# Optimization experiments

Hardware: AMD Instinct MI355X
Metric: run time of the kernel (lower is better)

Reference implementation:

```python
import jax, jax.numpy as jnp
import numpy as np

NUM_HEADS = 32
NUM_KV_HEADS = 8
HEAD_DIM = 128


def rotate_half(x):
    half = x.shape[-1] // 2
    return jnp.concatenate([-x[..., half:], x[..., :half]], axis=-1)


def setup_inputs() -> dict:
    key = jax.random.key(0)
    ks = jax.random.split(key, 7)
    B, S, H = 2, 2048, 4096
    hidden_states = jax.random.normal(ks[0], (B, S, H), dtype=jnp.float32)
    # rope tables built from real frequencies for realism
    inv_freq = 1.0 / (10000.0 ** (jnp.arange(0, HEAD_DIM, 2, dtype=jnp.float32) / HEAD_DIM))
    pos = jnp.arange(S, dtype=jnp.float32)
    freqs = pos[:, None] * inv_freq[None, :]            # [S, HEAD_DIM//2]
    emb = jnp.concatenate([freqs, freqs], axis=-1)      # [S, HEAD_DIM]
    cos = jnp.broadcast_to(jnp.cos(emb)[None], (B, S, HEAD_DIM)).astype(jnp.float32)
    sin = jnp.broadcast_to(jnp.sin(emb)[None], (B, S, HEAD_DIM)).astype(jnp.float32)
    scale = 0.02
    wq = jax.random.normal(ks[1], (NUM_HEADS * HEAD_DIM, H), dtype=jnp.float32) * scale
    wk = jax.random.normal(ks[2], (NUM_KV_HEADS * HEAD_DIM, H), dtype=jnp.float32) * scale
    wv = jax.random.normal(ks[3], (NUM_KV_HEADS * HEAD_DIM, H), dtype=jnp.float32) * scale
    wo = jax.random.normal(ks[4], (H, NUM_HEADS * HEAD_DIM), dtype=jnp.float32) * scale
    return {"hidden_states": hidden_states, "cos": cos, "sin": sin,
            "wq": wq, "wk": wk, "wv": wv, "wo": wo}


def reference(hidden_states, cos, sin, wq, wk, wv, wo):
    B, S, H = hidden_states.shape
    groups = NUM_HEADS // NUM_KV_HEADS
    scaling = HEAD_DIM ** -0.5

    # QKV projections (nn.Linear, no bias -> x @ W^T)
    q = (hidden_states @ wq.T).reshape(B, S, NUM_HEADS, HEAD_DIM).transpose(0, 2, 1, 3)     # [B,Hq,S,D]
    k = (hidden_states @ wk.T).reshape(B, S, NUM_KV_HEADS, HEAD_DIM).transpose(0, 2, 1, 3)  # [B,Hk,S,D]
    v = (hidden_states @ wv.T).reshape(B, S, NUM_KV_HEADS, HEAD_DIM).transpose(0, 2, 1, 3)  # [B,Hk,S,D]

    # RoPE (HF apply_rotary_pos_emb: cos/sin unsqueezed over head axis)
    c = cos[:, None, :, :]  # [B,1,S,D]
    s = sin[:, None, :, :]
    q = q * c + rotate_half(q) * s
    k = k * c + rotate_half(k) * s

    # GQA: broadcast each KV head to its group of query heads
    k = jnp.repeat(k, groups, axis=1)  # [B,Hq,S,D]
    v = jnp.repeat(v, groups, axis=1)

    # causal SDPA
    scores = jnp.einsum('bhqd,bhkd->bhqk', q, k) * scaling
    causal = jnp.tril(jnp.ones((S, S), dtype=bool))
    neg = jnp.finfo(scores.dtype).min
    scores = jnp.where(causal[None, None], scores, neg)
    probs = jax.nn.softmax(scores, axis=-1)
    attn = jnp.einsum('bhqk,bhkd->bhqd', probs, v)      # [B,Hq,S,D]

    # merge heads + output projection
    attn = attn.transpose(0, 2, 1, 3).reshape(B, S, NUM_HEADS * HEAD_DIM)
    return attn @ wo.T
```

## Files before the change

### kernel.cpp

```cpp
#include <hip/hip_runtime.h>
#include <stdint.h>

typedef __bf16 bf16_t;
typedef __bf16 bf16x8 __attribute__((ext_vector_type(8)));
typedef __bf16 bf16x4 __attribute__((ext_vector_type(4)));
typedef __bf16 bf16x2 __attribute__((ext_vector_type(2)));
typedef float f32x4 __attribute__((ext_vector_type(4)));

#define S_LEN 2048
#define NH 32
#define NKV 8
#define HD 128
#define B_SZ 2
#define HID 4096
#define QKV_N 6144
#define INFF __builtin_inff()
#define QSCALE (0.08838834764831845f * 1.4426950408889634f)

__device__ __forceinline__ void gload_lds16(const void* g, void* l) {
    __builtin_amdgcn_global_load_lds(
        (const __attribute__((address_space(1))) void*)(uintptr_t)g,
        (__attribute__((address_space(3))) void*)(uint32_t)(uintptr_t)l,
        16, 0, 0);
}

__global__ __launch_bounds__(256) void f2b_kernel(const float4* __restrict__ in,
                                                  bf16x4* __restrict__ out, int n4) {
    int i = blockIdx.x * blockDim.x + threadIdx.x;
    if (i >= n4) return;
    float4 v = in[i];
    bf16x4 o = {(bf16_t)v.x, (bf16_t)v.y, (bf16_t)v.z, (bf16_t)v.w};
    out[i] = o;
}

#define SLOT_E 16384

#define GTILE(T, STAGE, VMW) do {                                                         \
    const int _sb = ((T) & 3) * SLOT_E;                                                   \
    const int _ss = (((T) + 3) & 3) * SLOT_E;                                             \
    bf16x8 af[8], bfr[2], bfs[2];                                                         \
    _Pragma("unroll") for (int i = 0; i < 8; ++i)                                         \
        af[i] = *(const bf16x8*)&lds[_sb + offA[i]];                                      \
    bfr[0] = *(const bf16x8*)&lds[_sb + 8192 + offB[0]];                                  \
    bfr[1] = *(const bf16x8*)&lds[_sb + 8192 + offB[1]];                                  \
    if (STAGE) {                                                                          \
        gload_lds16(sA0, &lds[_ss + ldsO0]); gload_lds16(sA1, &lds[_ss + ldsO1]);         \
        sA0 += 32; sA1 += 32;                                                             \
    }                                                                                     \
    __builtin_amdgcn_s_setprio(1);                                                        \
    _Pragma("unroll") for (int i = 0; i < 8; ++i) {                                       \
        acc[i][0] = __builtin_amdgcn_mfma_f32_16x16x32_bf16(af[i], bfr[0], acc[i][0], 0, 0, 0); \
        acc[i][1] = __builtin_amdgcn_mfma_f32_16x16x32_bf16(af[i], bfr[1], acc[i][1], 0, 0, 0); \
    }                                                                                     \
    __builtin_amdgcn_s_setprio(0);                                                        \
    bfs[0] = *(const bf16x8*)&lds[_sb + 8192 + offB[2]];                                  \
    bfs[1] = *(const bf16x8*)&lds[_sb + 8192 + offB[3]];                                  \
    if (STAGE) {                                                                          \
        gload_lds16(sB0, &lds[_ss + 8192 + ldsO0]); gload_lds16(sB1, &lds[_ss + 8192 + ldsO1]); \
        sB0 += 32; sB1 += 32;                                                             \
    }                                                                                     \
    __builtin_amdgcn_s_setprio(1);                                                        \
    _Pragma("unroll") for (int i = 0; i < 8; ++i) {                                       \
        acc[i][2] = __builtin_amdgcn_mfma_f32_16x16x32_bf16(af[i], bfs[0], acc[i][2], 0, 0, 0); \
        acc[i][3] = __builtin_amdgcn_mfma_f32_16x16x32_bf16(af[i], bfs[1], acc[i][3], 0, 0, 0); \
    }                                                                                     \
    __builtin_amdgcn_s_setprio(0);                                                        \
    if ((VMW) == 8)      asm volatile("s_waitcnt vmcnt(8)" ::: "memory");                 \
    else if ((VMW) == 4) asm volatile("s_waitcnt vmcnt(4)" ::: "memory");                 \
    else if ((VMW) == 0) asm volatile("s_waitcnt vmcnt(0)" ::: "memory");                 \
    __builtin_amdgcn_s_barrier();                                                         \
} while (0)

template<bool F32OUT>
__global__ __launch_bounds__(512) void gemm256(const bf16_t* __restrict__ A,
                                               const bf16_t* __restrict__ W,
                                               void* __restrict__ C0,
                                               void* __restrict__ C1,
                                               int ld0, int ld1,
                                               int Nloc, int ldAW, int Kloc) {
    __shared__ __align__(16) bf16_t lds[4 * SLOT_E];
    const int tid = threadIdx.x;
    const int lane = tid & 63;
    const int w = tid >> 6;
    const int wm = w >> 2, wn = w & 3;
    const int l15 = lane & 15, lg = lane >> 4;

    const int z = blockIdx.y;
    void* Cv = z ? C1 : C0;
    const int ldC = z ? ld1 : ld0;
    const int kOff = z * Kloc;

    const int nbx = Nloc >> 8;
    const int cpx = gridDim.x >> 3;
    const int bid = blockIdx.x;
    const int bid2 = (bid & 7) * cpx + (bid >> 3);
    const int m0 = (bid2 / nbx) * 256;
    const int n0 = (bid2 % nbx) * 256;

    const int c0 = tid, c1 = 512 + tid;
    const int rA0 = c0 >> 2, ch0 = (c0 & 3) ^ ((rA0 >> 1) & 3);
    const int rA1 = c1 >> 2, ch1 = (c1 & 3) ^ ((rA1 >> 1) & 3);
    const bf16_t* sA0 = A + (size_t)(m0 + rA0) * ldAW + kOff + ch0 * 8;
    const bf16_t* sA1 = A + (size_t)(m0 + rA1) * ldAW + kOff + ch1 * 8;
    const bf16_t* sB0 = W + (size_t)(n0 + rA0) * ldAW + kOff + ch0 * 8;
    const bf16_t* sB1 = W + (size_t)(n0 + rA1) * ldAW + kOff + ch1 * 8;
    const int ldsO0 = c0 * 8, ldsO1 = c1 * 8;

    int offA[8], offB[4];
    #pragma unroll
    for (int i = 0; i < 8; ++i) {
        int row = wm * 128 + i * 16 + l15;
        offA[i] = row * 32 + ((lg ^ ((row >> 1) & 3)) * 8);
    }
    #pragma unroll
    for (int j = 0; j < 4; ++j) {
        int row = wn * 64 + j * 16 + l15;
        offB[j] = row * 32 + ((lg ^ ((row >> 1) & 3)) * 8);
    }

    #pragma unroll
    for (int tt = 0; tt < 3; ++tt) {
        const int ss = tt * SLOT_E;
        gload_lds16(sA0, &lds[ss + ldsO0]); gload_lds16(sA1, &lds[ss + ldsO1]);
        gload_lds16(sB0, &lds[ss + 8192 + ldsO0]); gload_lds16(sB1, &lds[ss + 8192 + ldsO1]);
        sA0 += 32; sA1 += 32; sB0 += 32; sB1 += 32;
    }
    asm volatile("s_waitcnt vmcnt(8)" ::: "memory");
    __builtin_amdgcn_s_barrier();

    f32x4 acc[8][4] = {};
    const int NT = Kloc >> 5;
    int t = 0;
    for (; t < NT - 3; ++t) GTILE(t, true, 8);
    GTILE(NT - 3, false, 4);
    GTILE(NT - 2, false, 0);
    GTILE(NT - 1, false, -1);

    #pragma unroll
    for (int i = 0; i < 8; ++i)
        #pragma unroll
        for (int jn = 0; jn < 4; ++jn)
            #pragma unroll
            for (int r = 0; r < 4; ++r) {
                int m = m0 + wm * 128 + i * 16 + lg * 4 + r;
                int n = n0 + wn * 64 + jn * 16 + l15;
                float v = acc[i][jn][r];
                if (F32OUT) ((float*)Cv)[(size_t)m * ldC + n] = v;
                else        ((bf16_t*)Cv)[(size_t)m * ldC + n] = (bf16_t)v;
            }
}

__global__ __launch_bounds__(256) void rope_fuse(bf16_t* __restrict__ QKV,
                                                 const bf16_t* __restrict__ P1,
                                                 const float* __restrict__ cosb,
                                                 const float* __restrict__ sinb) {
    int tid = blockIdx.x * blockDim.x + threadIdx.x;
    int d = tid & 63;
    int hg = (tid >> 6) % 48;
    int bs = tid / (64 * 48);
    bf16_t* rowp;
    float x1, x2, posc = 1.f;
    if (hg < 32) {
        rowp = QKV + (size_t)bs * QKV_N + hg * HD;
        x1 = (float)rowp[d];
        x2 = (float)rowp[d + 64];
        posc = QSCALE;
    } else if (hg < 40) {
        int col = HID + (hg - 32) * HD;
        rowp = QKV + (size_t)bs * QKV_N + col;
        const bf16_t* pp = P1 + (size_t)bs * 2048 + (col - HID);
        x1 = (float)rowp[d] + (float)pp[d];
        x2 = (float)rowp[d + 64] + (float)pp[d + 64];
    } else {
        int col = HID + NKV * HD + (hg - 40) * HD;
        rowp = QKV + (size_t)bs * QKV_N + col;
        const bf16_t* pp = P1 + (size_t)bs * 2048 + (col - HID);
        rowp[d]      = (bf16_t)((float)rowp[d]      + (float)pp[d]);
        rowp[d + 64] = (bf16_t)((float)rowp[d + 64] + (float)pp[d + 64]);
        return;
    }
    float c1 = cosb[(size_t)bs * HD + d];
    float s1 = sinb[(size_t)bs * HD + d];
    float c2 = cosb[(size_t)bs * HD + d + 64];
    float s2 = sinb[(size_t)bs * HD + d + 64];
    rowp[d]      = (bf16_t)((x1 * c1 - x2 * s1) * posc);
    rowp[d + 64] = (bf16_t)((x2 * c2 + x1 * s2) * posc);
}

#define PITCH_P 72

__global__ __launch_bounds__(512) void attn_fwd(const bf16_t* __restrict__ QKV,
                                                bf16_t* __restrict__ O) {
    __shared__ __align__(16) bf16_t Kl[2][64 * 128];
    __shared__ __align__(16) bf16_t Vt[2][128 * 64];
    __shared__ __align__(16) bf16_t Pl[8][2][16 * PITCH_P];
    const int tid = threadIdx.x;
    const int lane = tid & 63;
    const int w = tid >> 6;
    const int l15 = lane & 15, lg = lane >> 4;
    const int pr = blockIdx.x, kvh = blockIdx.y, b = blockIdx.z;
    const int h = kvh * 4 + (w & 3);
    const int rg = w >> 2;

    int krow[2], kch[2];
    #pragma unroll
    for (int jj = 0; jj < 2; ++jj) { int q = jj * 512 + tid; krow[jj] = q >> 4; kch[jj] = q & 15; }
    const int k0v = (tid & 31) * 2;
    const int d0 = (tid >> 5) * 8;
    const int vci = k0v >> 3;
    const int vsub = k0v & 7;

    const bf16_t* Kb0 = QKV + (size_t)(b * S_LEN) * QKV_N + HID + kvh * HD;
    const bf16_t* Vb0 = QKV + (size_t)(b * S_LEN) * QKV_N + HID + NKV * HD + kvh * HD;
    bf16_t* Pl0 = Pl[w][0];
    bf16_t* Pl1 = Pl[w][1];

    for (int t = 0; t < 2; ++t) {
        const int qt = (t == 0) ? pr : (31 - pr);
        const int q0 = qt * 64;
        const int qb0 = q0 + rg * 32;
        const int qb1 = qb0 + 16;
        const int qrow0 = qb0 + l15, qrow1 = qb1 + l15;

        bf16x8 qf0[4], qf1[4];
        {
            const bf16_t* qp0 = QKV + (size_t)(b * S_LEN + qrow0) * QKV_N + h * HD;
            const bf16_t* qp1 = QKV + (size_t)(b * S_LEN + qrow1) * QKV_N + h * HD;
            #pragma unroll
            for (int c = 0; c < 4; ++c) {
                qf0[c] = *(const bf16x8*)&qp0[c * 32 + lg * 8];
                qf1[c] = *(const bf16x8*)&qp1[c * 32 + lg * 8];
            }
        }

        f32x4 acc0[8] = {}, acc1[8] = {};
        float mr0 = -INFF, lr0 = 0.f, mr1 = -INFF, lr1 = 0.f;
        const int nsteps = qt + 1;

        bf16x8 kst[2], vst[2];
        #pragma unroll
        for (int jj = 0; jj < 2; ++jj)
            kst[jj] = *(const bf16x8*)&Kb0[(size_t)krow[jj] * QKV_N + kch[jj] * 8];
        vst[0] = *(const bf16x8*)&Vb0[(size_t)(k0v + 0) * QKV_N + d0];
        vst[1] = *(const bf16x8*)&Vb0[(size_t)(k0v + 1) * QKV_N + d0];

        for (int st = 0; st < nsteps; ++st) {
            const int k0 = st * 64;
            const int p = st & 1;
            #pragma unroll
            for (int jj = 0; jj < 2; ++jj)
                *(bf16x8*)&Kl[p][krow[jj] * 128 + ((kch[jj] ^ (krow[jj] & 7)) * 8)] = kst[jj];
            #pragma unroll
            for (int j = 0; j < 8; ++j) {
                bf16x2 v2 = { vst[0][j], vst[1][j] };
                *(bf16x2*)&Vt[p][(d0 + j) * 64 + ((vci ^ j) << 3) + vsub] = v2;
            }
            __syncthreads();
            if (st + 1 < nsteps) {
                const bf16_t* Kb = Kb0 + (size_t)(k0 + 64) * QKV_N;
                const bf16_t* Vb = Vb0 + (size_t)(k0 + 64) * QKV_N;
                #pragma unroll
                for (int jj = 0; jj < 2; ++jj)
                    kst[jj] = *(const bf16x8*)&Kb[(size_t)krow[jj] * QKV_N + kch[jj] * 8];
                vst[0] = *(const bf16x8*)&Vb[(size_t)(k0v + 0) * QKV_N + d0];
                vst[1] = *(const bf16x8*)&Vb[(size_t)(k0v + 1) * QKV_N + d0];
            }
            f32x4 s0[4], s1[4];
            __builtin_amdgcn_s_setprio(1);
            #pragma unroll
            for (int nt = 0; nt < 4; ++nt) {
                s0[nt] = (f32x4){0.f, 0.f, 0.f, 0.f};
                s1[nt] = (f32x4){0.f, 0.f, 0.f, 0.f};
                const int row = nt * 16 + l15;
                const int rb = row * 128, key = row & 7;
                #pragma unroll
                for (int c = 0; c < 4; ++c) {
                    bf16x8 kf = *(const bf16x8*)&Kl[p][rb + (((c * 4 + lg) ^ key) * 8)];
                    s0[nt] = __builtin_amdgcn_mfma_f32_16x16x32_bf16(kf, qf0[c], s0[nt], 0, 0, 0);
                    s1[nt] = __builtin_amdgcn_mfma_f32_16x16x32_bf16(kf, qf1[c], s1[nt], 0, 0, 0);
                }
            }
            __builtin_amdgcn_s_setprio(0);
            if (k0 + 63 > qb0) {
                #pragma unroll
                for (int nt = 0; nt < 4; ++nt)
                    #pragma unroll
                    for (int r = 0; r < 4; ++r) {
                        int k = k0 + nt * 16 + lg * 4 + r;
                        if (k > qrow0) s0[nt][r] = -INFF;
                    }
            }
            if (k0 + 63 > qb1) {
                #pragma unroll
                for (int nt = 0; nt < 4; ++nt)
                    #pragma unroll
                    for (int r = 0; r < 4; ++r) {
                        int k = k0 + nt * 16 + lg * 4 + r;
                        if (k > qrow1) s1[nt][r] = -INFF;
                    }
            }
            {
                float ma = fmaxf(fmaxf(s0[0][0], s0[0][1]), fmaxf(s0[0][2], s0[0][3]));
                float mb = fmaxf(fmaxf(s0[1][0], s0[1][1]), fmaxf(s0[1][2], s0[1][3]));
                float mc = fmaxf(fmaxf(s0[2][0], s0[2][1]), fmaxf(s0[2][2], s0[2][3]));
                float md = fmaxf(fmaxf(s0[3][0], s0[3][1]), fmaxf(s0[3][2], s0[3][3]));
                float mx = fmaxf(fmaxf(ma, mb), fmaxf(mc, md));
                mx = fmaxf(mx, __shfl_xor(mx, 16));
                mx = fmaxf(mx, __shfl_xor(mx, 32));
                const bool nodefer = !__all(mx <= mr0 + 11.5f);
                const float mn = nodefer ? fmaxf(mr0, mx) : mr0;
                float sc = 1.f;
                if (nodefer) sc = exp2f(mr0 - mn);
                float rsum = 0.f;
                #pragma unroll
                for (int nt = 0; nt < 4; ++nt) {
                    float e0 = exp2f(s0[nt][0] - mn), e1 = exp2f(s0[nt][1] - mn);
                    float e2 = exp2f(s0[nt][2] - mn), e3 = exp2f(s0[nt][3] - mn);
                    s0[nt][0] = e0; s0[nt][1] = e1; s0[nt][2] = e2; s0[nt][3] = e3;
                    rsum += (e0 + e1) + (e2 + e3);
                }
                rsum += __shfl_xor(rsum, 16);
                rsum += __shfl_xor(rsum, 32);
                if (nodefer) { lr0 = lr0 * sc + rsum; mr0 = mn; }
                else         { lr0 += rsum; }
                #pragma unroll
                for (int nt = 0; nt < 4; ++nt) {
                    bf16x4 pk = {(bf16_t)s0[nt][0], (bf16_t)s0[nt][1], (bf16_t)s0[nt][2], (bf16_t)s0[nt][3]};
                    *(bf16x4*)&Pl0[l15 * PITCH_P + nt * 16 + lg * 4] = pk;
                }
                if (nodefer) {
                    float scb[4];
                    #pragma unroll
                    for (int r = 0; r < 4; ++r) scb[r] = __shfl(sc, lg * 4 + r);
                    #pragma unroll
                    for (int nt2 = 0; nt2 < 8; ++nt2)
                        #pragma unroll
                        for (int r = 0; r < 4; ++r) acc0[nt2][r] *= scb[r];
                }
            }
            {
                float ma = fmaxf(fmaxf(s1[0][0], s1[0][1]), fmaxf(s1[0][2], s1[0][3]));
                float mb = fmaxf(fmaxf(s1[1][0], s1[1][1]), fmaxf(s1[1][2], s1[1][3]));
                float mc = fmaxf(fmaxf(s1[2][0], s1[2][1]), fmaxf(s1[2][2], s1[2][3]));
                float md = fmaxf(fmaxf(s1[3][0], s1[3][1]), fmaxf(s1[3][2], s1[3][3]));
                float mx = fmaxf(fmaxf(ma, mb), fmaxf(mc, md));
                mx = fmaxf(mx, __shfl_xor(mx, 16));
                mx = fmaxf(mx, __shfl_xor(mx, 32));
                const bool nodefer = !__all(mx <= mr1 + 11.5f);
                const float mn = nodefer ? fmaxf(mr1, mx) : mr1;
                float sc = 1.f;
                if (nodefer) sc = exp2f(mr1 - mn);
                float rsum = 0.f;
                #pragma unroll
                for (int nt = 0; nt < 4; ++nt) {
                    float e0 = exp2f(s1[nt][0] - mn), e1 = exp2f(s1[nt][1] - mn);
                    float e2 = exp2f(s1[nt][2] - mn), e3 = exp2f(s1[nt][3] - mn);
                    s1[nt][0] = e0; s1[nt][1] = e1; s1[nt][2] = e2; s1[nt][3] = e3;
                    rsum += (e0 + e1) + (e2 + e3);
                }
                rsum += __shfl_xor(rsum, 16);
                rsum += __shfl_xor(rsum, 32);
                if (nodefer) { lr1 = lr1 * sc + rsum; mr1 = mn; }
                else         { lr1 += rsum; }
                #pragma unroll
                for (int nt = 0; nt < 4; ++nt) {
                    bf16x4 pk = {(bf16_t)s1[nt][0], (bf16_t)s1[nt][1], (bf16_t)s1[nt][2], (bf16_t)s1[nt][3]};
                    *(bf16x4*)&Pl1[l15 * PITCH_P + nt * 16 + lg * 4] = pk;
                }
                if (nodefer) {
                    float scb[4];
                    #pragma unroll
                    for (int r = 0; r < 4; ++r) scb[r] = __shfl(sc, lg * 4 + r);
                    #pragma unroll
                    for (int nt2 = 0; nt2 < 8; ++nt2)
                        #pragma unroll
                        for (int r = 0; r < 4; ++r) acc1[nt2][r] *= scb[r];
                }
            }
            __builtin_amdgcn_s_setprio(1);
            #pragma unroll
            for (int kc = 0; kc < 2; ++kc) {
                bf16x8 pf0 = *(const bf16x8*)&Pl0[l15 * PITCH_P + kc * 32 + lg * 8];
                bf16x8 pf1 = *(const bf16x8*)&Pl1[l15 * PITCH_P + kc * 32 + lg * 8];
                #pragma unroll
                for (int nt2 = 0; nt2 < 8; ++nt2) {
                    const int drow = nt2 * 16 + l15;
                    bf16x8 vf = *(const bf16x8*)&Vt[p][drow * 64 + (((kc * 4 + lg) ^ (drow & 7)) << 3)];
                    acc0[nt2] = __builtin_amdgcn_mfma_f32_16x16x32_bf16(pf0, vf, acc0[nt2], 0, 0, 0);
                    acc1[nt2] = __builtin_amdgcn_mfma_f32_16x16x32_bf16(pf1, vf, acc1[nt2], 0, 0, 0);
                }
            }
            __builtin_amdgcn_s_setprio(0);
        }
        float lb0[4], lb1[4];
        #pragma unroll
        for (int r = 0; r < 4; ++r) {
            lb0[r] = __builtin_amdgcn_rcpf(__shfl(lr0, lg * 4 + r));
            lb1[r] = __builtin_amdgcn_rcpf(__shfl(lr1, lg * 4 + r));
        }
        #pragma unroll
        for (int nt2 = 0; nt2 < 8; ++nt2)
            #pragma unroll
            for (int r = 0; r < 4; ++r) {
                int d = nt2 * 16 + l15;
                int qa = qb0 + lg * 4 + r;
                int qb = qb1 + lg * 4 + r;
                O[((size_t)(b * S_LEN + qa)) * (NH * HD) + h * HD + d] = (bf16_t)(acc0[nt2][r] * lb0[r]);
                O[((size_t)(b * S_LEN + qb)) * (NH * HD) + h * HD + d] = (bf16_t)(acc1[nt2][r] * lb1[r]);
            }
        __syncthreads();
    }
}

extern "C" void kernel_launch(void* const* d_in, const int* in_sizes, int n_in,
                              void* d_out, int out_size, void* d_ws, size_t ws_size,
                              hipStream_t stream) {
    const float* hs   = (const float*)d_in[0];
    const float* cosb = (const float*)d_in[1];
    const float* sinb = (const float*)d_in[2];
    const float* wq   = (const float*)d_in[3];
    const float* wk   = (const float*)d_in[4];
    const float* wv   = (const float*)d_in[5];
    const float* wo   = (const float*)d_in[6];
    float* out = (float*)d_out;

    const size_t NHS = (size_t)B_SZ * S_LEN * HID;
    const size_t NQKVW = (size_t)QKV_N * HID;
    size_t need = (NHS * 3 + NQKVW * 2) * sizeof(bf16_t);
    if (ws_size < need) return;

    bf16_t* p = (bf16_t*)d_ws;
    bf16_t* hsb  = p; p += NHS;
    bf16_t* wqkv = p; p += NQKVW;
    bf16_t* wob  = p; p += NHS;
    bf16_t* QKVb = p; p += NQKVW;
    bf16_t* Ab   = p; p += NHS;
    bf16_t* P1   = Ab;

    auto cvt = [&](const float* src, bf16_t* dst, size_t n) {
        int n4 = (int)(n / 4);
        f2b_kernel<<<(n4 + 255) / 256, 256, 0, stream>>>((const float4*)src, (bf16x4*)dst, n4);
    };
    cvt(hs, hsb, NHS);
    cvt(wq, wqkv, NHS);
    cvt(wk, wqkv + (size_t)HID * HID, (size_t)NKV * HD * HID);
    cvt(wv, wqkv + (size_t)(HID + NKV * HD) * HID, (size_t)NKV * HD * HID);
    cvt(wo, wob, NHS);

    gemm256<false><<<dim3(256, 1), 512, 0, stream>>>(hsb, wqkv, QKVb, QKVb,
                                                     QKV_N, QKV_N, 4096, HID, HID);
    gemm256<false><<<dim3(128, 2), 512, 0, stream>>>(hsb, wqkv + (size_t)HID * HID,
                                                     QKVb + HID, P1,
                                                     QKV_N, 2048, 2048, HID, 2048);

    int rf_threads = B_SZ * S_LEN * 48 * 64;
    rope_fuse<<<rf_threads / 256, 256, 0, stream>>>(QKVb, P1, cosb, sinb);

    attn_fwd<<<dim3(16, NKV, B_SZ), 512, 0, stream>>>(QKVb, Ab);

    gemm256<true><<<dim3(256, 1), 512, 0, stream>>>(Ab, wob, out, out,
                                                    HID, HID, HID, HID, HID);
}
```

Baseline: 519.1 us.

## Split attention blocks into half-GQA-group blocks and XOR-swizzle the P tile

Each attention block now serves two of the four query heads in a KV group with 256 threads instead of all four with 512. The grid doubles to 512 blocks. Each thread loads more K/V rows per step, and V is transposed into LDS with 4-wide stores. The P scratch tile drops its padded pitch in favour of an XOR swizzle, which cuts LDS use per block. The goal is more blocks and better occupancy on the CUs, at the cost of each K/V tile being loaded twice (once per half-group).

```diff
diff --git a/kernel.cpp b/kernel.cpp
--- a/kernel.cpp
+++ b/kernel.cpp
@@ -187,26 +187,27 @@
     rowp[d + 64] = (bf16_t)((x2 * c2 + x1 * s2) * posc);
 }
 
-#define PITCH_P 72
-
-__global__ __launch_bounds__(512) void attn_fwd(const bf16_t* __restrict__ QKV,
+__global__ __launch_bounds__(256) void attn_fwd(const bf16_t* __restrict__ QKV,
                                                 bf16_t* __restrict__ O) {
     __shared__ __align__(16) bf16_t Kl[2][64 * 128];
     __shared__ __align__(16) bf16_t Vt[2][128 * 64];
-    __shared__ __align__(16) bf16_t Pl[8][2][16 * PITCH_P];
+    __shared__ __align__(16) bf16_t Pl[4][2][16 * 64];
     const int tid = threadIdx.x;
     const int lane = tid & 63;
     const int w = tid >> 6;
     const int l15 = lane & 15, lg = lane >> 4;
-    const int pr = blockIdx.x, kvh = blockIdx.y, b = blockIdx.z;
-    const int h = kvh * 4 + (w & 3);
-    const int rg = w >> 2;
-
-    int krow[2], kch[2];
+    const int pr = blockIdx.x;
+    const int kvh = blockIdx.y >> 1, hs = blockIdx.y & 1;
+    const int b = blockIdx.z;
+    const int h = kvh * 4 + hs * 2 + (w & 1);
+    const int rg = w >> 1;
+    const int pkey = l15 & 7;
+
+    int krow[4], kch[4];
     #pragma unroll
-    for (int jj = 0; jj < 2; ++jj) { int q = jj * 512 + tid; krow[jj] = q >> 4; kch[jj] = q & 15; }
-    const int k0v = (tid & 31) * 2;
-    const int d0 = (tid >> 5) * 8;
+    for (int jj = 0; jj < 4; ++jj) { int q = jj * 256 + tid; krow[jj] = q >> 4; kch[jj] = q & 15; }
+    const int k0v = (tid & 15) * 4;
+    const int d0 = (tid >> 4) * 8;
     const int vci = k0v >> 3;
     const int vsub = k0v & 7;
 
@@ -237,33 +238,35 @@
         float mr0 = -INFF, lr0 = 0.f, mr1 = -INFF, lr1 = 0.f;
         const int nsteps = qt + 1;
 
-        bf16x8 kst[2], vst[2];
+        bf16x8 kst[4], vst[4];
         #pragma unroll
-        for (int jj = 0; jj < 2; ++jj)
+        for (int jj = 0; jj < 4; ++jj)
             kst[jj] = *(const bf16x8*)&Kb0[(size_t)krow[jj] * QKV_N + kch[jj] * 8];
-        vst[0] = *(const bf16x8*)&Vb0[(size_t)(k0v + 0) * QKV_N + d0];
-        vst[1] = *(const bf16x8*)&Vb0[(size_t)(k0v + 1) * QKV_N + d0];
+        #pragma unroll
+        for (int j2 = 0; j2 < 4; ++j2)
+            vst[j2] = *(const bf16x8*)&Vb0[(size_t)(k0v + j2) * QKV_N + d0];
 
         for (int st = 0; st < nsteps; ++st) {
             const int k0 = st * 64;
             const int p = st & 1;
             #pragma unroll
-            for (int jj = 0; jj < 2; ++jj)
+            for (int jj = 0; jj < 4; ++jj)
                 *(bf16x8*)&Kl[p][krow[jj] * 128 + ((kch[jj] ^ (krow[jj] & 7)) * 8)] = kst[jj];
             #pragma unroll
             for (int j = 0; j < 8; ++j) {
-                bf16x2 v2 = { vst[0][j], vst[1][j] };
-                *(bf16x2*)&Vt[p][(d0 + j) * 64 + ((vci ^ j) << 3) + vsub] = v2;
+                bf16x4 cvec = { vst[0][j], vst[1][j], vst[2][j], vst[3][j] };
+                *(bf16x4*)&Vt[p][(d0 + j) * 64 + ((vci ^ j) << 3) + vsub] = cvec;
             }
             __syncthreads();
             if (st + 1 < nsteps) {
                 const bf16_t* Kb = Kb0 + (size_t)(k0 + 64) * QKV_N;
                 const bf16_t* Vb = Vb0 + (size_t)(k0 + 64) * QKV_N;
                 #pragma unroll
-                for (int jj = 0; jj < 2; ++jj)
+                for (int jj = 0; jj < 4; ++jj)
                     kst[jj] = *(const bf16x8*)&Kb[(size_t)krow[jj] * QKV_N + kch[jj] * 8];
-                vst[0] = *(const bf16x8*)&Vb[(size_t)(k0v + 0) * QKV_N + d0];
-                vst[1] = *(const bf16x8*)&Vb[(size_t)(k0v + 1) * QKV_N + d0];
+                #pragma unroll
+                for (int j2 = 0; j2 < 4; ++j2)
+                    vst[j2] = *(const bf16x8*)&Vb[(size_t)(k0v + j2) * QKV_N + d0];
             }
             f32x4 s0[4], s1[4];
             __builtin_amdgcn_s_setprio(1);
@@ -326,7 +329,8 @@
                 #pragma unroll
                 for (int nt = 0; nt < 4; ++nt) {
                     bf16x4 pk = {(bf16_t)s0[nt][0], (bf16_t)s0[nt][1], (bf16_t)s0[nt][2], (bf16_t)s0[nt][3]};
-                    *(bf16x4*)&Pl0[l15 * PITCH_P + nt * 16 + lg * 4] = pk;
+                    const int cw = nt * 2 + (lg >> 1);
+                    *(bf16x4*)&Pl0[l15 * 64 + ((cw ^ pkey) * 8) + (lg & 1) * 4] = pk;
                 }
                 if (nodefer) {
                     float scb[4];
@@ -365,7 +369,8 @@
                 #pragma unroll
                 for (int nt = 0; nt < 4; ++nt) {
                     bf16x4 pk = {(bf16_t)s1[nt][0], (bf16_t)s1[nt][1], (bf16_t)s1[nt][2], (bf16_t)s1[nt][3]};
-                    *(bf16x4*)&Pl1[l15 * PITCH_P + nt * 16 + lg * 4] = pk;
+                    const int cw = nt * 2 + (lg >> 1);
+                    *(bf16x4*)&Pl1[l15 * 64 + ((cw ^ pkey) * 8) + (lg & 1) * 4] = pk;
                 }
                 if (nodefer) {
                     float scb[4];
@@ -380,8 +385,8 @@
             __builtin_amdgcn_s_setprio(1);
             #pragma unroll
             for (int kc = 0; kc < 2; ++kc) {
-                bf16x8 pf0 = *(const bf16x8*)&Pl0[l15 * PITCH_P + kc * 32 + lg * 8];
-                bf16x8 pf1 = *(const bf16x8*)&Pl1[l15 * PITCH_P + kc * 32 + lg * 8];
+                bf16x8 pf0 = *(const bf16x8*)&Pl0[l15 * 64 + (((kc * 4 + lg) ^ pkey) * 8)];
+                bf16x8 pf1 = *(const bf16x8*)&Pl1[l15 * 64 + (((kc * 4 + lg) ^ pkey) * 8)];
                 #pragma unroll
                 for (int nt2 = 0; nt2 < 8; ++nt2) {
                     const int drow = nt2 * 16 + l15;
@@ -456,7 +461,7 @@
     int rf_threads = B_SZ * S_LEN * 48 * 64;
     rope_fuse<<<rf_threads / 256, 256, 0, stream>>>(QKVb, P1, cosb, sinb);
 
-    attn_fwd<<<dim3(16, NKV, B_SZ), 512, 0, stream>>>(QKVb, Ab);
+    attn_fwd<<<dim3(16, 16, B_SZ), 256, 0, stream>>>(QKVb, Ab);
 
     gemm256<true><<<dim3(256, 1), 512, 0, stream>>>(Ab, wob, out, out,
                                                     HID, HID, HID, HID, HID);
```

New measurement: 587.7 us. +13.2%, slower.

## Split attention blocks by head pair and shrink KV tile to 32 keys

Applied to the files above, without the earlier changes.

Each attention workgroup now covers two of the four query heads sharing a KV head, so the grid doubles to 512 blocks of 256 threads. The KV step shrinks from 64 to 32 keys, halving the K, V and P shared-memory tiles, and the swizzle patterns are adjusted to the narrower tiles. The aim is more blocks and smaller LDS per block for better occupancy and CU fill. In exchange each K/V tile is loaded by two blocks instead of one, and twice as many loop steps each carry a barrier and softmax bookkeeping.

```diff
diff --git a/kernel.cpp b/kernel.cpp
--- a/kernel.cpp
+++ b/kernel.cpp
@@ -187,26 +187,28 @@
     rowp[d + 64] = (bf16_t)((x2 * c2 + x1 * s2) * posc);
 }
 
-#define PITCH_P 72
-
-__global__ __launch_bounds__(512) void attn_fwd(const bf16_t* __restrict__ QKV,
+#define PITCH_P 40
+
+__global__ __launch_bounds__(256) void attn_fwd(const bf16_t* __restrict__ QKV,
                                                 bf16_t* __restrict__ O) {
-    __shared__ __align__(16) bf16_t Kl[2][64 * 128];
-    __shared__ __align__(16) bf16_t Vt[2][128 * 64];
-    __shared__ __align__(16) bf16_t Pl[8][2][16 * PITCH_P];
+    __shared__ __align__(16) bf16_t Kl[2][32 * 128];
+    __shared__ __align__(16) bf16_t Vt[2][128 * 32];
+    __shared__ __align__(16) bf16_t Pl[4][2][16 * PITCH_P];
     const int tid = threadIdx.x;
     const int lane = tid & 63;
     const int w = tid >> 6;
     const int l15 = lane & 15, lg = lane >> 4;
-    const int pr = blockIdx.x, kvh = blockIdx.y, b = blockIdx.z;
-    const int h = kvh * 4 + (w & 3);
-    const int rg = w >> 2;
+    const int pr = blockIdx.x;
+    const int kvh = blockIdx.y >> 1, hs = blockIdx.y & 1;
+    const int b = blockIdx.z;
+    const int h = kvh * 4 + hs * 2 + (w & 1);
+    const int rg = w >> 1;
 
     int krow[2], kch[2];
     #pragma unroll
-    for (int jj = 0; jj < 2; ++jj) { int q = jj * 512 + tid; krow[jj] = q >> 4; kch[jj] = q & 15; }
-    const int k0v = (tid & 31) * 2;
-    const int d0 = (tid >> 5) * 8;
+    for (int jj = 0; jj < 2; ++jj) { int q = jj * 256 + tid; krow[jj] = q >> 4; kch[jj] = q & 15; }
+    const int k0v = (tid & 15) * 2;
+    const int d0 = (tid >> 4) * 8;
     const int vci = k0v >> 3;
     const int vsub = k0v & 7;
 
@@ -235,7 +237,7 @@
 
         f32x4 acc0[8] = {}, acc1[8] = {};
         float mr0 = -INFF, lr0 = 0.f, mr1 = -INFF, lr1 = 0.f;
-        const int nsteps = qt + 1;
+        const int nsteps = 2 * qt + 2;
 
         bf16x8 kst[2], vst[2];
         #pragma unroll
@@ -245,7 +247,7 @@
         vst[1] = *(const bf16x8*)&Vb0[(size_t)(k0v + 1) * QKV_N + d0];
 
         for (int st = 0; st < nsteps; ++st) {
-            const int k0 = st * 64;
+            const int k0 = st * 32;
             const int p = st & 1;
             #pragma unroll
             for (int jj = 0; jj < 2; ++jj)
@@ -253,22 +255,23 @@
             #pragma unroll
             for (int j = 0; j < 8; ++j) {
                 bf16x2 v2 = { vst[0][j], vst[1][j] };
-                *(bf16x2*)&Vt[p][(d0 + j) * 64 + ((vci ^ j) << 3) + vsub] = v2;
+                const int d = d0 + j;
+                *(bf16x2*)&Vt[p][d * 32 + ((vci ^ (d & 3)) * 8) + vsub] = v2;
             }
             __syncthreads();
             if (st + 1 < nsteps) {
-                const bf16_t* Kb = Kb0 + (size_t)(k0 + 64) * QKV_N;
-                const bf16_t* Vb = Vb0 + (size_t)(k0 + 64) * QKV_N;
+                const bf16_t* Kb = Kb0 + (size_t)(k0 + 32) * QKV_N;
+                const bf16_t* Vb = Vb0 + (size_t)(k0 + 32) * QKV_N;
                 #pragma unroll
                 for (int jj = 0; jj < 2; ++jj)
                     kst[jj] = *(const bf16x8*)&Kb[(size_t)krow[jj] * QKV_N + kch[jj] * 8];
                 vst[0] = *(const bf16x8*)&Vb[(size_t)(k0v + 0) * QKV_N + d0];
                 vst[1] = *(const bf16x8*)&Vb[(size_t)(k0v + 1) * QKV_N + d0];
             }
-            f32x4 s0[4], s1[4];
+            f32x4 s0[2], s1[2];
             __builtin_amdgcn_s_setprio(1);
             #pragma unroll
-            for (int nt = 0; nt < 4; ++nt) {
+            for (int nt = 0; nt < 2; ++nt) {
                 s0[nt] = (f32x4){0.f, 0.f, 0.f, 0.f};
                 s1[nt] = (f32x4){0.f, 0.f, 0.f, 0.f};
                 const int row = nt * 16 + l15;
@@ -281,18 +284,18 @@
                 }
             }
             __builtin_amdgcn_s_setprio(0);
-            if (k0 + 63 > qb0) {
-                #pragma unroll
-                for (int nt = 0; nt < 4; ++nt)
+            if (k0 + 31 > qb0) {
+                #pragma unroll
+                for (int nt = 0; nt < 2; ++nt)
                     #pragma unroll
                     for (int r = 0; r < 4; ++r) {
                         int k = k0 + nt * 16 + lg * 4 + r;
                         if (k > qrow0) s0[nt][r] = -INFF;
                     }
             }
-            if (k0 + 63 > qb1) {
-                #pragma unroll
-                for (int nt = 0; nt < 4; ++nt)
+            if (k0 + 31 > qb1) {
+                #pragma unroll
+                for (int nt = 0; nt < 2; ++nt)
                     #pragma unroll
                     for (int r = 0; r < 4; ++r) {
                         int k = k0 + nt * 16 + lg * 4 + r;
@@ -302,9 +305,7 @@
             {
                 float ma = fmaxf(fmaxf(s0[0][0], s0[0][1]), fmaxf(s0[0][2], s0[0][3]));
                 float mb = fmaxf(fmaxf(s0[1][0], s0[1][1]), fmaxf(s0[1][2], s0[1][3]));
-                float mc = fmaxf(fmaxf(s0[2][0], s0[2][1]), fmaxf(s0[2][2], s0[2][3]));
-                float md = fmaxf(fmaxf(s0[3][0], s0[3][1]), fmaxf(s0[3][2], s0[3][3]));
-                float mx = fmaxf(fmaxf(ma, mb), fmaxf(mc, md));
+                float mx = fmaxf(ma, mb);
                 mx = fmaxf(mx, __shfl_xor(mx, 16));
                 mx = fmaxf(mx, __shfl_xor(mx, 32));
                 const bool nodefer = !__all(mx <= mr0 + 11.5f);
@@ -313,7 +314,7 @@
                 if (nodefer) sc = exp2f(mr0 - mn);
                 float rsum = 0.f;
                 #pragma unroll
-                for (int nt = 0; nt < 4; ++nt) {
+                for (int nt = 0; nt < 2; ++nt) {
                     float e0 = exp2f(s0[nt][0] - mn), e1 = exp2f(s0[nt][1] - mn);
                     float e2 = exp2f(s0[nt][2] - mn), e3 = exp2f(s0[nt][3] - mn);
                     s0[nt][0] = e0; s0[nt][1] = e1; s0[nt][2] = e2; s0[nt][3] = e3;
@@ -324,7 +325,7 @@
                 if (nodefer) { lr0 = lr0 * sc + rsum; mr0 = mn; }
                 else         { lr0 += rsum; }
                 #pragma unroll
-                for (int nt = 0; nt < 4; ++nt) {
+                for (int nt = 0; nt < 2; ++nt) {
                     bf16x4 pk = {(bf16_t)s0[nt][0], (bf16_t)s0[nt][1], (bf16_t)s0[nt][2], (bf16_t)s0[nt][3]};
                     *(bf16x4*)&Pl0[l15 * PITCH_P + nt * 16 + lg * 4] = pk;
                 }
@@ -341,9 +342,7 @@
             {
                 float ma = fmaxf(fmaxf(s1[0][0], s1[0][1]), fmaxf(s1[0][2], s1[0][3]));
                 float mb = fmaxf(fmaxf(s1[1][0], s1[1][1]), fmaxf(s1[1][2], s1[1][3]));
-                float mc = fmaxf(fmaxf(s1[2][0], s1[2][1]), fmaxf(s1[2][2], s1[2][3]));
-                float md = fmaxf(fmaxf(s1[3][0], s1[3][1]), fmaxf(s1[3][2], s1[3][3]));
-                float mx = fmaxf(fmaxf(ma, mb), fmaxf(mc, md));
+                float mx = fmaxf(ma, mb);
                 mx = fmaxf(mx, __shfl_xor(mx, 16));
                 mx = fmaxf(mx, __shfl_xor(mx, 32));
                 const bool nodefer = !__all(mx <= mr1 + 11.5f);
@@ -352,7 +351,7 @@
                 if (nodefer) sc = exp2f(mr1 - mn);
                 float rsum = 0.f;
                 #pragma unroll
-                for (int nt = 0; nt < 4; ++nt) {
+                for (int nt = 0; nt < 2; ++nt) {
                     float e0 = exp2f(s1[nt][0] - mn), e1 = exp2f(s1[nt][1] - mn);
                     float e2 = exp2f(s1[nt][2] - mn), e3 = exp2f(s1[nt][3] - mn);
                     s1[nt][0] = e0; s1[nt][1] = e1; s1[nt][2] = e2; s1[nt][3] = e3;
@@ -363,7 +362,7 @@
                 if (nodefer) { lr1 = lr1 * sc + rsum; mr1 = mn; }
                 else         { lr1 += rsum; }
                 #pragma unroll
-                for (int nt = 0; nt < 4; ++nt) {
+                for (int nt = 0; nt < 2; ++nt) {
                     bf16x4 pk = {(bf16_t)s1[nt][0], (bf16_t)s1[nt][1], (bf16_t)s1[nt][2], (bf16_t)s1[nt][3]};
                     *(bf16x4*)&Pl1[l15 * PITCH_P + nt * 16 + lg * 4] = pk;
                 }
@@ -378,14 +377,13 @@
                 }
             }
             __builtin_amdgcn_s_setprio(1);
-            #pragma unroll
-            for (int kc = 0; kc < 2; ++kc) {
-                bf16x8 pf0 = *(const bf16x8*)&Pl0[l15 * PITCH_P + kc * 32 + lg * 8];
-                bf16x8 pf1 = *(const bf16x8*)&Pl1[l15 * PITCH_P + kc * 32 + lg * 8];
+            {
+                bf16x8 pf0 = *(const bf16x8*)&Pl0[l15 * PITCH_P + lg * 8];
+                bf16x8 pf1 = *(const bf16x8*)&Pl1[l15 * PITCH_P + lg * 8];
                 #pragma unroll
                 for (int nt2 = 0; nt2 < 8; ++nt2) {
                     const int drow = nt2 * 16 + l15;
-                    bf16x8 vf = *(const bf16x8*)&Vt[p][drow * 64 + (((kc * 4 + lg) ^ (drow & 7)) << 3)];
+                    bf16x8 vf = *(const bf16x8*)&Vt[p][drow * 32 + ((lg ^ (drow & 3)) * 8)];
                     acc0[nt2] = __builtin_amdgcn_mfma_f32_16x16x32_bf16(pf0, vf, acc0[nt2], 0, 0, 0);
                     acc1[nt2] = __builtin_amdgcn_mfma_f32_16x16x32_bf16(pf1, vf, acc1[nt2], 0, 0, 0);
                 }
@@ -456,7 +454,7 @@
     int rf_threads = B_SZ * S_LEN * 48 * 64;
     rope_fuse<<<rf_threads / 256, 256, 0, stream>>>(QKVb, P1, cosb, sinb);
 
-    attn_fwd<<<dim3(16, NKV, B_SZ), 512, 0, stream>>>(QKVb, Ab);
+    attn_fwd<<<dim3(16, 16, B_SZ), 256, 0, stream>>>(QKVb, Ab);
 
     gemm256<true><<<dim3(256, 1), 512, 0, stream>>>(Ab, wob, out, out,
                                                     HID, HID, HID, HID, HID);
```

Result: slower. 619.8 us (+19.4%).
